# Performance work log

Measured on AMD Instinct MI355X. Metric: run time of the kernel, lower is better.

## Reference

```python
import jax, jax.numpy as jnp
import numpy as np

B, C_IN, H, W = 1024, 3, 32, 32
D_IN = C_IN * H * W          # 3072, matches input_size
R_HID = 128                  # router hidden_size
E = 8                        # num experts
TOP_K = 2
E_HID = 2048                 # expert MLP hidden
N_CLS = 10                   # cifar classes


def setup_inputs() -> dict:
    key = jax.random.key(0)
    ks = jax.random.split(key, 10)
    s = lambda fan_in: 1.0 / np.sqrt(fan_in)
    x = jax.random.normal(ks[0], (B, C_IN, H, W), jnp.float32)
    # router params
    rW1 = jax.random.normal(ks[1], (D_IN, R_HID), jnp.float32) * s(D_IN)
    rb1 = jnp.zeros((R_HID,), jnp.float32)
    rW2 = jax.random.normal(ks[2], (R_HID, E), jnp.float32) * s(R_HID)
    rb2 = jnp.zeros((E,), jnp.float32)
    # stacked expert params [E, ...]
    eW1 = jax.random.normal(ks[3], (E, D_IN, E_HID), jnp.float32) * s(D_IN)
    eb1 = jnp.zeros((E, E_HID), jnp.float32)
    eW2 = jax.random.normal(ks[4], (E, E_HID, N_CLS), jnp.float32) * s(E_HID)
    eb2 = jnp.zeros((E, N_CLS), jnp.float32)
    return {"x": x, "rW1": rW1, "rb1": rb1, "rW2": rW2, "rb2": rb2,
            "eW1": eW1, "eb1": eb1, "eW2": eW2, "eb2": eb2}


def reference(x, rW1, rb1, rW2, rb2, eW1, eb1, eW2, eb2):
    b = x.shape[0]
    xf = x.reshape(b, -1)                                  # [B, D_IN]
    # router (eval mode: no noise, no dropout)
    rh = jax.nn.relu(xf @ rW1 + rb1)
    logits = rh @ rW2 + rb2                                # [B, E]
    rw = jax.nn.softmax(logits, axis=-1)
    w, idx = jax.lax.top_k(rw, TOP_K)                      # [B, K]
    w = w / jnp.sum(w, axis=-1, keepdims=True)
    # dense per-expert compute (same math as masked dispatch)
    eh = jax.nn.relu(jnp.einsum('bd,edh->ebh', xf, eW1) + eb1[:, None, :])  # [E,B,H]
    outs = jnp.einsum('ebh,ehc->ebc', eh, eW2) + eb2[:, None, :]            # [E,B,C]
    # combine: gather each sample's top-k expert outputs
    taken = outs[idx.T, jnp.arange(b)[None, :]]            # [K, B, C]
    return jnp.sum(w.T[:, :, None] * taken, axis=0)        # [B, C]
```

## Files before the change

### kernel.cpp

```cpp
#include <hip/hip_runtime.h>
#include <cstdint>
#include <cstddef>

#define B_TOK 1024
#define DD_IN 3072
#define RHID 128
#define NEXP 8
#define EHID 2048
#define NCLS 10

typedef __attribute__((ext_vector_type(8))) short short8;
typedef __attribute__((ext_vector_type(4))) float floatx4;

__device__ __forceinline__ unsigned short f2bf(float f) {
  unsigned u = __builtin_bit_cast(unsigned, f);
  u += 0x7fffu + ((u >> 16) & 1u);
  return (unsigned short)(u >> 16);
}
__device__ __forceinline__ unsigned pk_bf16(float a, float b) {
  return (unsigned)f2bf(a) | ((unsigned)f2bf(b) << 16);
}
__device__ __forceinline__ float bf2f(unsigned short h) {
  unsigned u = ((unsigned)h) << 16;
  return __builtin_bit_cast(float, u);
}
__device__ __forceinline__ void gload16(const void* g, void* l) {
  __builtin_amdgcn_global_load_lds((const __attribute__((address_space(1))) void*)g,
                                   (__attribute__((address_space(3))) void*)l, 16, 0, 0);
}

__global__ __launch_bounds__(256) void k_router_gemm(const float* __restrict__ x,
                                                     const float* __restrict__ rW1,
                                                     float* __restrict__ partial,
                                                     unsigned short* __restrict__ xbf,
                                                     int* __restrict__ cnt) {
  if (blockIdx.x == 0 && blockIdx.y == 0 && threadIdx.x < NEXP) cnt[threadIdx.x] = 0;
  const int ttile = blockIdx.x;
  const int s = blockIdx.y;
  const int T0 = ttile * 64;
  const int K0 = s * 192;
  __shared__ float xs[16][64];
  __shared__ float wsm[16][132];
  float acc[4][8];
#pragma unroll
  for (int i = 0; i < 4; i++)
#pragma unroll
    for (int j = 0; j < 8; j++) acc[i][j] = 0.f;
  const int tx = threadIdx.x & 15, ty = threadIdx.x >> 4;
  const int tid = threadIdx.x;

  const int xtok = tid >> 2, xk = (tid & 3) << 2;
  const int wk0 = tid >> 5, wf0 = (tid & 31) << 2;

  float4 pX, pW0, pW1;
  pX  = *(const float4*)(x + (size_t)(T0 + xtok) * DD_IN + K0 + xk);
  pW0 = *(const float4*)(rW1 + (size_t)(K0 + wk0) * RHID + wf0);
  pW1 = *(const float4*)(rW1 + (size_t)(K0 + wk0 + 8) * RHID + wf0);

  for (int kc = K0; kc < K0 + 192; kc += 16) {
    xs[xk + 0][xtok] = pX.x; xs[xk + 1][xtok] = pX.y;
    xs[xk + 2][xtok] = pX.z; xs[xk + 3][xtok] = pX.w;
    {
      uint2 xw;
      xw.x = pk_bf16(pX.x, pX.y);
      xw.y = pk_bf16(pX.z, pX.w);
      *(uint2*)(xbf + (size_t)(T0 + xtok) * DD_IN + kc + xk) = xw;
    }
    *(float4*)&wsm[wk0][wf0] = pW0;
    *(float4*)&wsm[wk0 + 8][wf0] = pW1;
    __syncthreads();
    if (kc + 16 < K0 + 192) {
      pX  = *(const float4*)(x + (size_t)(T0 + xtok) * DD_IN + kc + 16 + xk);
      pW0 = *(const float4*)(rW1 + (size_t)(kc + 16 + wk0) * RHID + wf0);
      pW1 = *(const float4*)(rW1 + (size_t)(kc + 16 + wk0 + 8) * RHID + wf0);
    }
#pragma unroll
    for (int kk = 0; kk < 16; kk++) {
      float wv[8], xv[4];
      *(float4*)&wv[0] = *(const float4*)&wsm[kk][tx * 8];
      *(float4*)&wv[4] = *(const float4*)&wsm[kk][tx * 8 + 4];
#pragma unroll
      for (int i = 0; i < 4; i++) xv[i] = xs[kk][ty * 4 + i];
#pragma unroll
      for (int i = 0; i < 4; i++)
#pragma unroll
        for (int j = 0; j < 8; j++) acc[i][j] += xv[i] * wv[j];
    }
    __syncthreads();
  }
#pragma unroll
  for (int i = 0; i < 4; i++) {
    float* p = partial + ((size_t)s * B_TOK + T0 + ty * 4 + i) * RHID + tx * 8;
    *(float4*)p = *(float4*)&acc[i][0];
    *(float4*)(p + 4) = *(float4*)&acc[i][4];
  }
}

__global__ __launch_bounds__(256) void k_router_fin(const float* __restrict__ partial,
                                                    const float* __restrict__ rb1,
                                                    const float* __restrict__ rW2,
                                                    const float* __restrict__ rb2,
                                                    const float* __restrict__ eb2,
                                                    float* __restrict__ out,
                                                    int* __restrict__ cnt,
                                                    int* __restrict__ tokL,
                                                    float* __restrict__ wtL) {
  if (threadIdx.x < 4 * NCLS)
    out[blockIdx.x * 4 * NCLS + threadIdx.x] = eb2[threadIdx.x % NCLS];
  const int lane = threadIdx.x & 63;
  const int tok = blockIdx.x * 4 + (threadIdx.x >> 6);
  float r0 = 0.f, r1 = 0.f;
#pragma unroll
  for (int s = 0; s < 16; s++) {
    const float* p = partial + ((size_t)s * B_TOK + tok) * RHID;
    r0 += p[lane]; r1 += p[lane + 64];
  }
  r0 = fmaxf(r0 + rb1[lane], 0.f);
  r1 = fmaxf(r1 + rb1[lane + 64], 0.f);
  float lg[8];
#pragma unroll
  for (int c = 0; c < 8; c++)
    lg[c] = r0 * rW2[lane * 8 + c] + r1 * rW2[(lane + 64) * 8 + c];
#pragma unroll
  for (int off = 32; off >= 1; off >>= 1)
#pragma unroll
    for (int c = 0; c < 8; c++) lg[c] += __shfl_down(lg[c], off);
  if (lane == 0) {
    float m1 = -1e30f, m2 = -1e30f; int i1 = 0, i2 = 0;
#pragma unroll
    for (int c = 0; c < 8; c++) {
      float l = lg[c] + rb2[c];
      if (l > m1) { m2 = m1; i2 = i1; m1 = l; i1 = c; }
      else if (l > m2) { m2 = l; i2 = c; }
    }
    float w1 = 1.f / (1.f + expf(m2 - m1));
    float w2 = 1.f - w1;
    int p1 = atomicAdd(&cnt[i1], 1);
    tokL[i1 * B_TOK + p1] = tok; wtL[i1 * B_TOK + p1] = w1;
    int p2 = atomicAdd(&cnt[i2], 1);
    tokL[i2 * B_TOK + p2] = tok; wtL[i2 * B_TOK + p2] = w2;
  }
}

#define ISSUE_B(s_) do { _Pragma("unroll") for (int i_ = 0; i_ < 2; i_++) { \
    sBa[s_][i_] = *(const float4*)pB[i_]; \
    sBb[s_][i_] = *(const float4*)(pB[i_] + EHID); \
    pB[i_] += (size_t)64 * EHID; } } while (0)

#define ISSUE_A(p_) do { _Pragma("unroll") for (int i_ = 0; i_ < 4; i_++) { \
    gload16((const void*)srcA[i_], (void*)&u.a.As[p_][i_ * 32 + w8][0]); \
    srcA[i_] += 64; } } while (0)

#define CONV_B(s_) do { _Pragma("unroll") for (int i_ = 0; i_ < 2; i_++) { \
    uint4 wv_; \
    wv_.x = pk_bf16(sBa[s_][i_].x, sBb[s_][i_].x); \
    wv_.y = pk_bf16(sBa[s_][i_].y, sBb[s_][i_].y); \
    wv_.z = pk_bf16(sBa[s_][i_].z, sBb[s_][i_].z); \
    wv_.w = pk_bf16(sBa[s_][i_].w, sBb[s_][i_].w); \
    int br_ = brow + i_ * 16; \
    *(uint4*)&u.a.Bs[br_][bcol ^ (((br_ >> 2) & 1) << 4)] = wv_; } } while (0)

#define PIPE_SYNC(N_) do { \
    asm volatile("s_waitcnt vmcnt(" #N_ ") lgkmcnt(0)" ::: "memory"); \
    __builtin_amdgcn_sched_barrier(0); \
    __builtin_amdgcn_s_barrier(); \
    __builtin_amdgcn_sched_barrier(0); } while (0)

#define END_BAR do { \
    __builtin_amdgcn_sched_barrier(0); \
    __builtin_amdgcn_s_barrier(); \
    __builtin_amdgcn_sched_barrier(0); } while (0)

#define MFMA_PH(p_) do { \
  _Pragma("unroll") for (int kk = 0; kk < 2; kk++) { \
    short8 af[4], bfr[2]; \
    _Pragma("unroll") for (int mi = 0; mi < 4; mi++) { \
      int row_ = wm + mi * 16 + col; \
      int cs_ = (kk * 4 + quad) ^ (row_ & 7); \
      af[mi] = *(const short8*)((const char*)&u.a.As[p_][0][0] + row_ * 128 + (cs_ << 4)); \
    } \
    _Pragma("unroll") for (int ni = 0; ni < 2; ni++) { \
      int kb_ = kk * 16 + quad * 4; \
      int nb_ = (wn + ni * 16 + col) ^ ((quad & 1) << 4); \
      uint4 t_; \
      t_.x = u.a.Bs[kb_ + 0][nb_]; t_.y = u.a.Bs[kb_ + 1][nb_]; \
      t_.z = u.a.Bs[kb_ + 2][nb_]; t_.w = u.a.Bs[kb_ + 3][nb_]; \
      bfr[ni] = __builtin_bit_cast(short8, t_); \
    } \
    _Pragma("unroll") for (int mi = 0; mi < 4; mi++) \
      _Pragma("unroll") for (int ni = 0; ni < 2; ni++) \
        acc[mi][ni] = __builtin_amdgcn_mfma_f32_16x16x32_bf16(af[mi], bfr[ni], acc[mi][ni], 0, 0, 0); \
  } } while (0)

__global__ __launch_bounds__(256, 3) void k_expert(const unsigned short* __restrict__ xbf,
                                                   const float* __restrict__ eW1,
                                                   const float* __restrict__ eb1,
                                                   const float* __restrict__ eW2,
                                                   const int* __restrict__ cnt,
                                                   const int* __restrict__ tokL,
                                                   const float* __restrict__ wtL,
                                                   float* __restrict__ out) {
  const int nt = blockIdx.x;
  int mt = blockIdx.y;
  int e = 0;
#pragma unroll
  for (e = 0; e < NEXP; e++) {
    int te = (cnt[e] + 127) >> 7;
    if (mt < te) break;
    mt -= te;
  }
  if (e >= NEXP) return;
  const int cnt_e = cnt[e];

  __shared__ union {
    struct { unsigned short As[2][128][64]; unsigned Bs[32][64]; } a;
    struct { unsigned short ehs[128][68]; float w2[64 * NCLS]; } b;
  } u;
  __shared__ int stok[128];
  __shared__ float swt[128];

  const int tid = threadIdx.x;
  if (tid < 128) {
    int r = mt * 128 + tid;
    bool v = r < cnt_e;
    stok[tid] = v ? tokL[e * B_TOK + r] : -1;
    swt[tid]  = v ? wtL[e * B_TOK + r] : 0.f;
  }
  __syncthreads();

  const int lane = tid & 63;
  const int wv = tid >> 6;
  const int w8 = wv << 3;
  const int wm = (wv >> 1) << 6, wn = (wv & 1) << 5;
  const int col = lane & 15, quad = lane >> 4;

  floatx4 acc[4][2];
#pragma unroll
  for (int mi = 0; mi < 4; mi++)
#pragma unroll
    for (int ni = 0; ni < 2; ni++) acc[mi][ni] = (floatx4)0.f;

  const int r8 = tid >> 3, c16 = tid & 7;
  const int c16s = c16 ^ (r8 & 7);
  const unsigned short* srcA[4];
#pragma unroll
  for (int i = 0; i < 4; i++) {
    int tk = stok[r8 + i * 32];
    if (tk < 0) tk = 0;
    srcA[i] = xbf + (size_t)tk * DD_IN + (c16s << 3);
  }
  const float* W1e = eW1 + (size_t)e * DD_IN * EHID + (size_t)nt * 64;
  const int brow = tid >> 4, bcol = (tid & 15) << 2;
  const float* pB[2];
#pragma unroll
  for (int i = 0; i < 2; i++) pB[i] = W1e + (size_t)(2 * (brow + i * 16)) * EHID + bcol;

  float4 sBa[2][2], sBb[2][2];

  ISSUE_B(0);
  ISSUE_A(0);

  for (int t = 0; t < 48; t += 2) {
    ISSUE_B(1); ISSUE_A(1);
    CONV_B(0);
    PIPE_SYNC(8);
    MFMA_PH(0);
    END_BAR;
    if (t < 46) {
      ISSUE_B(0); ISSUE_A(0);
      CONV_B(1);
      PIPE_SYNC(8);
    } else {
      CONV_B(1);
      PIPE_SYNC(0);
    }
    MFMA_PH(1);
    END_BAR;
  }

#pragma unroll
  for (int ni = 0; ni < 2; ni++) {
    int hid = wn + ni * 16 + col;
    float bias = eb1[(size_t)e * EHID + nt * 64 + hid];
#pragma unroll
    for (int mi = 0; mi < 4; mi++)
#pragma unroll
      for (int r = 0; r < 4; r++) {
        float val = fmaxf(acc[mi][ni][r] + bias, 0.f);
        u.b.ehs[wm + mi * 16 + quad * 4 + r][hid] = f2bf(val);
      }
  }
#pragma unroll
  for (int i = 0; i < 3; i++) {
    int idx = tid + i * 256;
    if (idx < 64 * NCLS)
      u.b.w2[idx] = eW2[((size_t)e * EHID + nt * 64 + idx / NCLS) * NCLS + (idx % NCLS)];
  }
  __syncthreads();
  {
    int tok = tid >> 1, half = tid & 1;
    float a10[NCLS];
#pragma unroll
    for (int c = 0; c < NCLS; c++) a10[c] = 0.f;
    for (int hh = 0; hh < 32; hh++) {
      int h = half * 32 + hh;
      float eh = bf2f(u.b.ehs[tok][h]);
#pragma unroll
      for (int c = 0; c < NCLS; c++) a10[c] += eh * u.b.w2[h * NCLS + c];
    }
#pragma unroll
    for (int c = 0; c < NCLS; c++) a10[c] += __shfl_xor(a10[c], 1);
    int tk = stok[tok];
    if (half == 0 && tk >= 0) {
      float wt = swt[tok];
#pragma unroll
      for (int c = 0; c < NCLS; c++)
        atomicAdd(out + (size_t)tk * NCLS + c, wt * a10[c]);
    }
  }
}

extern "C" void kernel_launch(void* const* d_in, const int* in_sizes, int n_in,
                              void* d_out, int out_size, void* d_ws, size_t ws_size,
                              hipStream_t stream) {
  const float* x   = (const float*)d_in[0];
  const float* rW1 = (const float*)d_in[1];
  const float* rb1 = (const float*)d_in[2];
  const float* rW2 = (const float*)d_in[3];
  const float* rb2 = (const float*)d_in[4];
  const float* eW1 = (const float*)d_in[5];
  const float* eb1 = (const float*)d_in[6];
  const float* eW2 = (const float*)d_in[7];
  const float* eb2 = (const float*)d_in[8];
  float* out = (float*)d_out;

  char* ws = (char*)d_ws;
  int*   cnt     = (int*)(ws + 0);
  int*   tokL    = (int*)(ws + 1024);
  float* wtL     = (float*)(ws + 33792);
  float* partial = (float*)(ws + 66560);
  unsigned short* xbf = (unsigned short*)(ws + 66560 + (size_t)16 * B_TOK * RHID * 4);

  k_router_gemm<<<dim3(16, 16), 256, 0, stream>>>(x, rW1, partial, xbf, cnt);
  k_router_fin<<<256, 256, 0, stream>>>(partial, rb1, rW2, rb2, eb2, out, cnt, tokL, wtL);
  k_expert<<<dim3(32, 24), 256, 0, stream>>>(xbf, eW1, eb1, eW2, cnt, tokL, wtL, out);
}
```

Measured before the change: 423.3 us.

## Halve expert N-tile to 32 and deepen weight prefetch to three stages

Shrinks the expert GEMM N tile from 64 to 32 hidden units, which doubles the grid in x and cuts per-thread accumulators and LDS. Occupancy is raised to 4 blocks per CU. The fp32 weight register prefetch becomes a three-slot rotation so B loads are issued two phases ahead, with an unrolled six-phase loop and an explicit tail. The trade-off is that each block re-reads the gathered bf16 activation tile for half as many output columns, doubling A traffic, and issues twice as many output atomics.

```diff
diff --git a/kernel.cpp b/kernel.cpp
--- a/kernel.cpp
+++ b/kernel.cpp
@@ -142,23 +142,22 @@
   }
 }
 
-#define ISSUE_B(s_) do { _Pragma("unroll") for (int i_ = 0; i_ < 2; i_++) { \
-    sBa[s_][i_] = *(const float4*)pB[i_]; \
-    sBb[s_][i_] = *(const float4*)(pB[i_] + EHID); \
-    pB[i_] += (size_t)64 * EHID; } } while (0)
+#define ISSUE_B(s_) do { \
+    sBa[s_] = *(const float4*)pB; \
+    sBb[s_] = *(const float4*)(pB + EHID); \
+    pB += (size_t)64 * EHID; } while (0)
 
 #define ISSUE_A(p_) do { _Pragma("unroll") for (int i_ = 0; i_ < 4; i_++) { \
     gload16((const void*)srcA[i_], (void*)&u.a.As[p_][i_ * 32 + w8][0]); \
     srcA[i_] += 64; } } while (0)
 
-#define CONV_B(s_) do { _Pragma("unroll") for (int i_ = 0; i_ < 2; i_++) { \
+#define CONV_B(s_) do { \
     uint4 wv_; \
-    wv_.x = pk_bf16(sBa[s_][i_].x, sBb[s_][i_].x); \
-    wv_.y = pk_bf16(sBa[s_][i_].y, sBb[s_][i_].y); \
-    wv_.z = pk_bf16(sBa[s_][i_].z, sBb[s_][i_].z); \
-    wv_.w = pk_bf16(sBa[s_][i_].w, sBb[s_][i_].w); \
-    int br_ = brow + i_ * 16; \
-    *(uint4*)&u.a.Bs[br_][bcol ^ (((br_ >> 2) & 1) << 4)] = wv_; } } while (0)
+    wv_.x = pk_bf16(sBa[s_].x, sBb[s_].x); \
+    wv_.y = pk_bf16(sBa[s_].y, sBb[s_].y); \
+    wv_.z = pk_bf16(sBa[s_].z, sBb[s_].z); \
+    wv_.w = pk_bf16(sBa[s_].w, sBb[s_].w); \
+    *(uint4*)&u.a.Bs[brow][bcol4 ^ (((brow >> 2) & 1) << 4)] = wv_; } while (0)
 
 #define PIPE_SYNC(N_) do { \
     asm volatile("s_waitcnt vmcnt(" #N_ ") lgkmcnt(0)" ::: "memory"); \
@@ -173,26 +172,33 @@
 
 #define MFMA_PH(p_) do { \
   _Pragma("unroll") for (int kk = 0; kk < 2; kk++) { \
-    short8 af[4], bfr[2]; \
+    short8 af[4], bfr; \
     _Pragma("unroll") for (int mi = 0; mi < 4; mi++) { \
       int row_ = wm + mi * 16 + col; \
       int cs_ = (kk * 4 + quad) ^ (row_ & 7); \
       af[mi] = *(const short8*)((const char*)&u.a.As[p_][0][0] + row_ * 128 + (cs_ << 4)); \
     } \
-    _Pragma("unroll") for (int ni = 0; ni < 2; ni++) { \
+    { \
       int kb_ = kk * 16 + quad * 4; \
-      int nb_ = (wn + ni * 16 + col) ^ ((quad & 1) << 4); \
+      int nb_ = (wn + col) ^ ((quad & 1) << 4); \
       uint4 t_; \
       t_.x = u.a.Bs[kb_ + 0][nb_]; t_.y = u.a.Bs[kb_ + 1][nb_]; \
       t_.z = u.a.Bs[kb_ + 2][nb_]; t_.w = u.a.Bs[kb_ + 3][nb_]; \
-      bfr[ni] = __builtin_bit_cast(short8, t_); \
+      bfr = __builtin_bit_cast(short8, t_); \
     } \
     _Pragma("unroll") for (int mi = 0; mi < 4; mi++) \
-      _Pragma("unroll") for (int ni = 0; ni < 2; ni++) \
-        acc[mi][ni] = __builtin_amdgcn_mfma_f32_16x16x32_bf16(af[mi], bfr[ni], acc[mi][ni], 0, 0, 0); \
+      acc[mi] = __builtin_amdgcn_mfma_f32_16x16x32_bf16(af[mi], bfr, acc[mi], 0, 0, 0); \
   } } while (0)
 
-__global__ __launch_bounds__(256, 3) void k_expert(const unsigned short* __restrict__ xbf,
+#define PH(s_, s2_, ab_) do { \
+    ISSUE_A(ab_ ^ 1); \
+    ISSUE_B(s2_); \
+    CONV_B(s_); \
+    PIPE_SYNC(8); \
+    MFMA_PH(ab_); \
+    END_BAR; } while (0)
+
+__global__ __launch_bounds__(256, 4) void k_expert(const unsigned short* __restrict__ xbf,
                                                    const float* __restrict__ eW1,
                                                    const float* __restrict__ eb1,
                                                    const float* __restrict__ eW2,
@@ -213,8 +219,8 @@
   const int cnt_e = cnt[e];
 
   __shared__ union {
-    struct { unsigned short As[2][128][64]; unsigned Bs[32][64]; } a;
-    struct { unsigned short ehs[128][68]; float w2[64 * NCLS]; } b;
+    struct { unsigned short As[2][128][64]; unsigned Bs[32][32]; } a;
+    struct { unsigned short ehs[128][36]; float w2[32 * NCLS]; } b;
   } u;
   __shared__ int stok[128];
   __shared__ float swt[128];
@@ -231,14 +237,12 @@
   const int lane = tid & 63;
   const int wv = tid >> 6;
   const int w8 = wv << 3;
-  const int wm = (wv >> 1) << 6, wn = (wv & 1) << 5;
+  const int wm = (wv >> 1) << 6, wn = (wv & 1) << 4;
   const int col = lane & 15, quad = lane >> 4;
 
-  floatx4 acc[4][2];
-#pragma unroll
-  for (int mi = 0; mi < 4; mi++)
-#pragma unroll
-    for (int ni = 0; ni < 2; ni++) acc[mi][ni] = (floatx4)0.f;
+  floatx4 acc[4];
+#pragma unroll
+  for (int mi = 0; mi < 4; mi++) acc[mi] = (floatx4)0.f;
 
   const int r8 = tid >> 3, c16 = tid & 7;
   const int c16s = c16 ^ (r8 & 7);
@@ -249,52 +253,54 @@
     if (tk < 0) tk = 0;
     srcA[i] = xbf + (size_t)tk * DD_IN + (c16s << 3);
   }
-  const float* W1e = eW1 + (size_t)e * DD_IN * EHID + (size_t)nt * 64;
-  const int brow = tid >> 4, bcol = (tid & 15) << 2;
-  const float* pB[2];
-#pragma unroll
-  for (int i = 0; i < 2; i++) pB[i] = W1e + (size_t)(2 * (brow + i * 16)) * EHID + bcol;
-
-  float4 sBa[2][2], sBb[2][2];
+  const float* W1e = eW1 + (size_t)e * DD_IN * EHID + (size_t)nt * 32;
+  const int brow = tid >> 3, bcol4 = (tid & 7) << 2;
+  const float* pB = W1e + (size_t)(2 * brow) * EHID + bcol4;
+
+  float4 sBa[3], sBb[3];
 
   ISSUE_B(0);
   ISSUE_A(0);
-
-  for (int t = 0; t < 48; t += 2) {
-    ISSUE_B(1); ISSUE_A(1);
-    CONV_B(0);
-    PIPE_SYNC(8);
-    MFMA_PH(0);
-    END_BAR;
-    if (t < 46) {
-      ISSUE_B(0); ISSUE_A(0);
-      CONV_B(1);
-      PIPE_SYNC(8);
-    } else {
-      CONV_B(1);
-      PIPE_SYNC(0);
-    }
-    MFMA_PH(1);
-    END_BAR;
-  }
-
-#pragma unroll
-  for (int ni = 0; ni < 2; ni++) {
-    int hid = wn + ni * 16 + col;
-    float bias = eb1[(size_t)e * EHID + nt * 64 + hid];
+  ISSUE_B(1);
+
+  for (int t = 0; t < 42; t += 6) {
+    PH(0, 2, 0);
+    PH(1, 0, 1);
+    PH(2, 1, 0);
+    PH(0, 2, 1);
+    PH(1, 0, 0);
+    PH(2, 1, 1);
+  }
+  PH(0, 2, 0);
+  PH(1, 0, 1);
+  PH(2, 1, 0);
+  PH(0, 2, 1);
+  ISSUE_A(1);
+  CONV_B(1);
+  PIPE_SYNC(6);
+  MFMA_PH(0);
+  END_BAR;
+  CONV_B(2);
+  PIPE_SYNC(0);
+  MFMA_PH(1);
+  END_BAR;
+
+  {
+    int hid = wn + col;
+    float bias = eb1[(size_t)e * EHID + nt * 32 + hid];
 #pragma unroll
     for (int mi = 0; mi < 4; mi++)
 #pragma unroll
       for (int r = 0; r < 4; r++) {
-        float val = fmaxf(acc[mi][ni][r] + bias, 0.f);
+        float val = fmaxf(acc[mi][r] + bias, 0.f);
         u.b.ehs[wm + mi * 16 + quad * 4 + r][hid] = f2bf(val);
       }
   }
 #pragma unroll
-  for (int i = 0; i < 3; i++) {
+  for (int i = 0; i < 2; i++) {
     int idx = tid + i * 256;
-    if (idx < 64 * NCLS)
-      u.b.w2[idx] = eW2[((size_t)e * EHID + nt * 64 + idx / NCLS) * NCLS + (idx % NCLS)];
+    if (idx < 32 * NCLS)
+      u.b.w2[idx] = eW2[((size_t)e * EHID + nt * 32 + idx / NCLS) * NCLS + (idx % NCLS)];
   }
   __syncthreads();
   {
@@ -302,8 +308,8 @@
     float a10[NCLS];
 #pragma unroll
     for (int c = 0; c < NCLS; c++) a10[c] = 0.f;
-    for (int hh = 0; hh < 32; hh++) {
-      int h = half * 32 + hh;
+    for (int hh = 0; hh < 16; hh++) {
+      int h = half * 16 + hh;
       float eh = bf2f(u.b.ehs[tok][h]);
 #pragma unroll
       for (int c = 0; c < NCLS; c++) a10[c] += eh * u.b.w2[h * NCLS + c];
@@ -343,5 +349,5 @@
 
   k_router_gemm<<<dim3(16, 16), 256, 0, stream>>>(x, rW1, partial, xbf, cnt);
   k_router_fin<<<256, 256, 0, stream>>>(partial, rb1, rW2, rb2, eb2, out, cnt, tokL, wtL);
-  k_expert<<<dim3(32, 24), 256, 0, stream>>>(xbf, eW1, eb1, eW2, cnt, tokL, wtL, out);
-}
+  k_expert<<<dim3(64, 24), 256, 0, stream>>>(xbf, eW1, eb1, eW2, cnt, tokL, wtL, out);
+}
```

After: 537.2 us. 26.9% more time.

## Double-buffer B tile to drop per-phase end barrier, use hardware bf16 pack

Applied to the files above, without the earlier changes.

Adds a second LDS buffer for the converted B (weight) tile, so each phase needs only one barrier instead of two. The A global-to-LDS loads for the next stage are now issued after the sync, and the vmcnt wait is relaxed. The manual round-to-nearest bf16 packing is replaced by the v_cvt_pk_bf16_f32 instruction, and MFMA sections are wrapped in s_setprio. LDS use grows by 8KB per block, which could affect the three-blocks-per-CU occupancy target, and the reordered waits carry a correctness risk if the counts are off.

```diff
diff --git a/kernel.cpp b/kernel.cpp
--- a/kernel.cpp
+++ b/kernel.cpp
@@ -19,6 +19,11 @@
 }
 __device__ __forceinline__ unsigned pk_bf16(float a, float b) {
   return (unsigned)f2bf(a) | ((unsigned)f2bf(b) << 16);
+}
+__device__ __forceinline__ unsigned cvtpk(float lo, float hi) {
+  unsigned r;
+  asm("v_cvt_pk_bf16_f32 %0, %1, %2" : "=v"(r) : "v"(lo), "v"(hi));
+  return r;
 }
 __device__ __forceinline__ float bf2f(unsigned short h) {
   unsigned u = ((unsigned)h) << 16;
@@ -153,12 +158,12 @@
 
 #define CONV_B(s_) do { _Pragma("unroll") for (int i_ = 0; i_ < 2; i_++) { \
     uint4 wv_; \
-    wv_.x = pk_bf16(sBa[s_][i_].x, sBb[s_][i_].x); \
-    wv_.y = pk_bf16(sBa[s_][i_].y, sBb[s_][i_].y); \
-    wv_.z = pk_bf16(sBa[s_][i_].z, sBb[s_][i_].z); \
-    wv_.w = pk_bf16(sBa[s_][i_].w, sBb[s_][i_].w); \
+    wv_.x = cvtpk(sBa[s_][i_].x, sBb[s_][i_].x); \
+    wv_.y = cvtpk(sBa[s_][i_].y, sBb[s_][i_].y); \
+    wv_.z = cvtpk(sBa[s_][i_].z, sBb[s_][i_].z); \
+    wv_.w = cvtpk(sBa[s_][i_].w, sBb[s_][i_].w); \
     int br_ = brow + i_ * 16; \
-    *(uint4*)&u.a.Bs[br_][bcol ^ (((br_ >> 2) & 1) << 4)] = wv_; } } while (0)
+    *(uint4*)&u.a.Bs[s_][br_][bcol ^ (((br_ >> 2) & 1) << 4)] = wv_; } } while (0)
 
 #define PIPE_SYNC(N_) do { \
     asm volatile("s_waitcnt vmcnt(" #N_ ") lgkmcnt(0)" ::: "memory"); \
@@ -166,12 +171,8 @@
     __builtin_amdgcn_s_barrier(); \
     __builtin_amdgcn_sched_barrier(0); } while (0)
 
-#define END_BAR do { \
-    __builtin_amdgcn_sched_barrier(0); \
-    __builtin_amdgcn_s_barrier(); \
-    __builtin_amdgcn_sched_barrier(0); } while (0)
-
 #define MFMA_PH(p_) do { \
+  __builtin_amdgcn_s_setprio(1); \
   _Pragma("unroll") for (int kk = 0; kk < 2; kk++) { \
     short8 af[4], bfr[2]; \
     _Pragma("unroll") for (int mi = 0; mi < 4; mi++) { \
@@ -183,14 +184,22 @@
       int kb_ = kk * 16 + quad * 4; \
       int nb_ = (wn + ni * 16 + col) ^ ((quad & 1) << 4); \
       uint4 t_; \
-      t_.x = u.a.Bs[kb_ + 0][nb_]; t_.y = u.a.Bs[kb_ + 1][nb_]; \
-      t_.z = u.a.Bs[kb_ + 2][nb_]; t_.w = u.a.Bs[kb_ + 3][nb_]; \
+      t_.x = u.a.Bs[p_][kb_ + 0][nb_]; t_.y = u.a.Bs[p_][kb_ + 1][nb_]; \
+      t_.z = u.a.Bs[p_][kb_ + 2][nb_]; t_.w = u.a.Bs[p_][kb_ + 3][nb_]; \
       bfr[ni] = __builtin_bit_cast(short8, t_); \
     } \
     _Pragma("unroll") for (int mi = 0; mi < 4; mi++) \
       _Pragma("unroll") for (int ni = 0; ni < 2; ni++) \
         acc[mi][ni] = __builtin_amdgcn_mfma_f32_16x16x32_bf16(af[mi], bfr[ni], acc[mi][ni], 0, 0, 0); \
-  } } while (0)
+  } \
+  __builtin_amdgcn_s_setprio(0); } while (0)
+
+#define PH(par_) do { \
+    ISSUE_B(par_ ^ 1); \
+    CONV_B(par_); \
+    PIPE_SYNC(4); \
+    ISSUE_A(par_ ^ 1); \
+    MFMA_PH(par_); } while (0)
 
 __global__ __launch_bounds__(256, 3) void k_expert(const unsigned short* __restrict__ xbf,
                                                    const float* __restrict__ eW1,
@@ -213,7 +222,7 @@
   const int cnt_e = cnt[e];
 
   __shared__ union {
-    struct { unsigned short As[2][128][64]; unsigned Bs[32][64]; } a;
+    struct { unsigned short As[2][128][64]; unsigned Bs[2][32][64]; } a;
     struct { unsigned short ehs[128][68]; float w2[64 * NCLS]; } b;
   } u;
   __shared__ int stok[128];
@@ -260,23 +269,20 @@
   ISSUE_B(0);
   ISSUE_A(0);
 
-  for (int t = 0; t < 48; t += 2) {
-    ISSUE_B(1); ISSUE_A(1);
-    CONV_B(0);
-    PIPE_SYNC(8);
-    MFMA_PH(0);
-    END_BAR;
-    if (t < 46) {
-      ISSUE_B(0); ISSUE_A(0);
-      CONV_B(1);
-      PIPE_SYNC(8);
-    } else {
-      CONV_B(1);
-      PIPE_SYNC(0);
-    }
-    MFMA_PH(1);
-    END_BAR;
-  }
+  for (int t = 0; t < 46; t += 2) {
+    PH(0);
+    PH(1);
+  }
+  ISSUE_B(1);
+  CONV_B(0);
+  PIPE_SYNC(4);
+  ISSUE_A(1);
+  MFMA_PH(0);
+  CONV_B(1);
+  PIPE_SYNC(0);
+  MFMA_PH(1);
+
+  __syncthreads();
 
 #pragma unroll
   for (int ni = 0; ni < 2; ni++) {
```

Result: no change. 423.9 us (+0.2%).
